# Kernel optimization log

Measured on AMD Instinct MI355X. Metric: run time of the kernel, lower is better.

Reference implementation:

```python
import jax, jax.numpy as jnp
import numpy as np

CUTOFF = 1.0          # nm, PhysNet attenuation cutoff
KE = 138.96           # Coulomb constant in kJ/mol*nm/e^2
N_ATOMS = 245760
N_PAIRS = 16_777_216
N_MOLS = 4096


def physnet_attenuation(r):
    # PhysNet smooth cutoff: 1 - 6u^5 + 15u^4 - 10u^3 for u = r/cutoff < 1, else 0
    u = r / CUTOFF
    phi = 1.0 - 6.0 * u**5 + 15.0 * u**4 - 10.0 * u**3
    return jnp.where(u < 1.0, phi, 0.0)


def setup_inputs() -> dict:
    key = jax.random.key(0)
    k1, k2, k3, k4 = jax.random.split(key, 4)
    per_atom_charge = jax.random.normal(k1, (N_ATOMS,), dtype=jnp.float32) * 0.2
    raw = jax.random.randint(k2, (2, N_PAIRS), 0, N_ATOMS, dtype=jnp.int32)
    # enforce idx_i <= idx_j; equal pairs are dropped by the idx_i < idx_j mask
    pair_indices = jnp.stack([jnp.minimum(raw[0], raw[1]), jnp.maximum(raw[0], raw[1])])
    # distances in (0.05, 1.5) nm to avoid div-by-zero and span the cutoff
    d_ij = jax.random.uniform(k3, (N_PAIRS, 1), dtype=jnp.float32) * 1.45 + 0.05
    atomic_subsystem_indices = jax.random.randint(k4, (N_PAIRS,), 0, N_MOLS, dtype=jnp.int32)
    per_system_energy = jnp.zeros((N_MOLS,), dtype=jnp.float32)
    return {
        "per_atom_charge": per_atom_charge,
        "pair_indices": pair_indices,
        "d_ij": d_ij,
        "atomic_subsystem_indices": atomic_subsystem_indices,
        "per_system_energy": per_system_energy,
    }


def reference(per_atom_charge, pair_indices, d_ij, atomic_subsystem_indices, per_system_energy):
    idx_i = pair_indices[0]
    idx_j = pair_indices[1]
    unique_mask = idx_i < idx_j  # keep each pair once (static-shape masking via where)
    d = d_ij[:, 0]  # [P]
    phi_2r = physnet_attenuation(2.0 * d)
    # cutoff-blended Coulomb kernel chi(r)
    chi_r = phi_2r / jnp.sqrt(d * d + 1.0) + (1.0 - phi_2r) / d
    contrib = per_atom_charge[idx_i] * per_atom_charge[idx_j] * chi_r
    contrib = jnp.where(unique_mask, contrib, 0.0)
    energy = per_system_energy + jax.ops.segment_sum(
        contrib, atomic_subsystem_indices, num_segments=N_MOLS
    )
    return energy * KE
```

## Files before the change

### kernel.cpp

```cpp
#include <hip/hip_runtime.h>

static constexpr int   NPAIRS = 16777216;
static constexpr int   NMOLS  = 4096;
static constexpr float KEF    = 138.96f;
static constexpr int   TPB    = 256;
static constexpr int   BLOCKS = 2048;
static constexpr int   WAVES  = TPB / 64;
static constexpr int   NITER  = NPAIRS / 4 / (BLOCKS * TPB);

typedef int   vi4 __attribute__((ext_vector_type(4)));
typedef float vf4 __attribute__((ext_vector_type(4)));

__global__ __launch_bounds__(256) void zero_out_kernel(float* __restrict__ out) {
    int i = blockIdx.x * 256 + threadIdx.x;
    if (i < NMOLS) out[i] = 0.0f;
}

__device__ __forceinline__ void stage16(const void* gptr, void* lptr) {
    __builtin_amdgcn_global_load_lds((const unsigned int*)gptr, (unsigned int*)lptr,
                                     16, 0, 0);
}

__device__ __forceinline__ float pair_contrib(const float* __restrict__ q,
                                              int i, int j, float d) {
    float u = 2.0f * d;
    float phi = 0.0f;
    if (u < 1.0f) {
        phi = 1.0f - u * u * u * (10.0f + u * (6.0f * u - 15.0f));
    }
    float rs = __builtin_amdgcn_rsqf(d * d + 1.0f);
    float rd = __builtin_amdgcn_rcpf(d);
    float chi = phi * rs + (1.0f - phi) * rd;
    float c = q[i] * q[j] * chi;
    return (i < j) ? c : 0.0f;
}

__global__ __launch_bounds__(TPB) void coulomb_kernel(
    const float* __restrict__ q,
    const int*   __restrict__ pidx,
    const float* __restrict__ dij,
    const int*   __restrict__ mol,
    float*       __restrict__ out)
{
    __shared__ float bins[NMOLS];
    __shared__ vi4   stage[WAVES][4][64];
    for (int i = threadIdx.x; i < NMOLS; i += TPB) bins[i] = 0.0f;
    __syncthreads();

    const vi4* pi4 = (const vi4*)pidx;
    const vi4* pj4 = (const vi4*)(pidx + NPAIRS);
    const vf4* d4  = (const vf4*)dij;
    const vi4* m4  = (const vi4*)mol;

    const int lane   = threadIdx.x & 63;
    const int wave   = threadIdx.x >> 6;
    const int stride = BLOCKS * TPB;
    int v = blockIdx.x * TPB + threadIdx.x;

    #pragma unroll 1
    for (int k = 0; k < NITER; ++k, v += stride) {
        stage16(&pi4[v], &stage[wave][0][0]);
        stage16(&pj4[v], &stage[wave][1][0]);
        stage16(&d4[v],  &stage[wave][2][0]);
        stage16(&m4[v],  &stage[wave][3][0]);
        asm volatile("s_waitcnt vmcnt(0)" ::: "memory");

        vi4 ii = stage[wave][0][lane];
        vi4 jj = stage[wave][1][lane];
        vf4 dd = (vf4)stage[wave][2][lane];
        vi4 mm = stage[wave][3][lane];

        float c0 = pair_contrib(q, ii.x, jj.x, dd.x);
        float c1 = pair_contrib(q, ii.y, jj.y, dd.y);
        float c2 = pair_contrib(q, ii.z, jj.z, dd.z);
        float c3 = pair_contrib(q, ii.w, jj.w, dd.w);

        atomicAdd(&bins[mm.x], c0);
        atomicAdd(&bins[mm.y], c1);
        atomicAdd(&bins[mm.z], c2);
        atomicAdd(&bins[mm.w], c3);
    }

    __syncthreads();
    for (int i = threadIdx.x; i < NMOLS; i += TPB) {
        atomicAdd(&out[i], bins[i]);
    }
}

__global__ __launch_bounds__(256) void finalize_kernel(float* __restrict__ out,
                                                       const float* __restrict__ pse) {
    int i = blockIdx.x * 256 + threadIdx.x;
    if (i < NMOLS) out[i] = (out[i] + pse[i]) * KEF;
}

extern "C" void kernel_launch(void* const* d_in, const int* in_sizes, int n_in,
                              void* d_out, int out_size, void* d_ws, size_t ws_size,
                              hipStream_t stream) {
    const float* q    = (const float*)d_in[0];
    const int*   pidx = (const int*)  d_in[1];
    const float* dij  = (const float*)d_in[2];
    const int*   mol  = (const int*)  d_in[3];
    const float* pse  = (const float*)d_in[4];
    float* out = (float*)d_out;

    zero_out_kernel<<<NMOLS / 256, 256, 0, stream>>>(out);
    coulomb_kernel<<<BLOCKS, TPB, 0, stream>>>(q, pidx, dij, mol, out);
    finalize_kernel<<<NMOLS / 256, 256, 0, stream>>>(out, pse);
}
```

Measured before the change: 381.0 us.

## Software-pipeline register prefetch of pair streams, drop LDS staging, use 1024-thread blocks

Replaces the per-iteration global_load_lds staging with a full vmcnt(0) wait by register-based software pipelining. Index vectors are prefetched two iterations ahead and distances and molecule ids one iteration ahead, all with nontemporal loads. Block size goes from 256 to 1024 threads with 512 blocks, which cuts the number of per-block LDS histograms to merge. The aim is to overlap the dependent charge gathers with streaming loads, at the cost of higher register pressure and occupancy pressure from the launch_bounds hint.

Result: slower. 393.0 us (+3.2%).

```diff
diff --git a/kernel.cpp b/kernel.cpp
--- a/kernel.cpp
+++ b/kernel.cpp
@@ -3,9 +3,8 @@
 static constexpr int   NPAIRS = 16777216;
 static constexpr int   NMOLS  = 4096;
 static constexpr float KEF    = 138.96f;
-static constexpr int   TPB    = 256;
-static constexpr int   BLOCKS = 2048;
-static constexpr int   WAVES  = TPB / 64;
+static constexpr int   TPB    = 1024;
+static constexpr int   BLOCKS = 512;
 static constexpr int   NITER  = NPAIRS / 4 / (BLOCKS * TPB);
 
 typedef int   vi4 __attribute__((ext_vector_type(4)));
@@ -16,12 +15,7 @@
     if (i < NMOLS) out[i] = 0.0f;
 }
 
-__device__ __forceinline__ void stage16(const void* gptr, void* lptr) {
-    __builtin_amdgcn_global_load_lds((const unsigned int*)gptr, (unsigned int*)lptr,
-                                     16, 0, 0);
-}
-
-__device__ __forceinline__ float pair_contrib(const float* __restrict__ q,
+__device__ __forceinline__ float pair_contrib(float qi, float qj,
                                               int i, int j, float d) {
     float u = 2.0f * d;
     float phi = 0.0f;
@@ -31,11 +25,11 @@
     float rs = __builtin_amdgcn_rsqf(d * d + 1.0f);
     float rd = __builtin_amdgcn_rcpf(d);
     float chi = phi * rs + (1.0f - phi) * rd;
-    float c = q[i] * q[j] * chi;
+    float c = qi * qj * chi;
     return (i < j) ? c : 0.0f;
 }
 
-__global__ __launch_bounds__(TPB) void coulomb_kernel(
+__global__ __launch_bounds__(TPB, 8) void coulomb_kernel(
     const float* __restrict__ q,
     const int*   __restrict__ pidx,
     const float* __restrict__ dij,
@@ -43,7 +37,6 @@
     float*       __restrict__ out)
 {
     __shared__ float bins[NMOLS];
-    __shared__ vi4   stage[WAVES][4][64];
     for (int i = threadIdx.x; i < NMOLS; i += TPB) bins[i] = 0.0f;
     __syncthreads();
 
@@ -52,33 +45,49 @@
     const vf4* d4  = (const vf4*)dij;
     const vi4* m4  = (const vi4*)mol;
 
-    const int lane   = threadIdx.x & 63;
-    const int wave   = threadIdx.x >> 6;
     const int stride = BLOCKS * TPB;
     int v = blockIdx.x * TPB + threadIdx.x;
 
+    vi4 ii0 = __builtin_nontemporal_load(&pi4[v]);
+    vi4 jj0 = __builtin_nontemporal_load(&pj4[v]);
+    vi4 ii1 = __builtin_nontemporal_load(&pi4[v + stride]);
+    vi4 jj1 = __builtin_nontemporal_load(&pj4[v + stride]);
+    vf4 dd0 = __builtin_nontemporal_load(&d4[v]);
+    vi4 mm0 = __builtin_nontemporal_load(&m4[v]);
+
     #pragma unroll 1
-    for (int k = 0; k < NITER; ++k, v += stride) {
-        stage16(&pi4[v], &stage[wave][0][0]);
-        stage16(&pj4[v], &stage[wave][1][0]);
-        stage16(&d4[v],  &stage[wave][2][0]);
-        stage16(&m4[v],  &stage[wave][3][0]);
-        asm volatile("s_waitcnt vmcnt(0)" ::: "memory");
+    for (int k = 0; k < NITER; ++k) {
+        vi4 ii2 = ii1, jj2 = jj1;
+        vf4 dd1 = dd0;
+        vi4 mm1 = mm0;
+        if (k + 2 < NITER) {
+            ii2 = __builtin_nontemporal_load(&pi4[v + 2 * stride]);
+            jj2 = __builtin_nontemporal_load(&pj4[v + 2 * stride]);
+        }
+        if (k + 1 < NITER) {
+            dd1 = __builtin_nontemporal_load(&d4[v + stride]);
+            mm1 = __builtin_nontemporal_load(&m4[v + stride]);
+        }
 
-        vi4 ii = stage[wave][0][lane];
-        vi4 jj = stage[wave][1][lane];
-        vf4 dd = (vf4)stage[wave][2][lane];
-        vi4 mm = stage[wave][3][lane];
+        float qi0 = q[ii0.x], qj0 = q[jj0.x];
+        float qi1 = q[ii0.y], qj1 = q[jj0.y];
+        float qi2 = q[ii0.z], qj2 = q[jj0.z];
+        float qi3 = q[ii0.w], qj3 = q[jj0.w];
 
-        float c0 = pair_contrib(q, ii.x, jj.x, dd.x);
-        float c1 = pair_contrib(q, ii.y, jj.y, dd.y);
-        float c2 = pair_contrib(q, ii.z, jj.z, dd.z);
-        float c3 = pair_contrib(q, ii.w, jj.w, dd.w);
+        float c0 = pair_contrib(qi0, qj0, ii0.x, jj0.x, dd0.x);
+        float c1 = pair_contrib(qi1, qj1, ii0.y, jj0.y, dd0.y);
+        float c2 = pair_contrib(qi2, qj2, ii0.z, jj0.z, dd0.z);
+        float c3 = pair_contrib(qi3, qj3, ii0.w, jj0.w, dd0.w);
 
-        atomicAdd(&bins[mm.x], c0);
-        atomicAdd(&bins[mm.y], c1);
-        atomicAdd(&bins[mm.z], c2);
-        atomicAdd(&bins[mm.w], c3);
+        atomicAdd(&bins[mm0.x], c0);
+        atomicAdd(&bins[mm0.y], c1);
+        atomicAdd(&bins[mm0.z], c2);
+        atomicAdd(&bins[mm0.w], c3);
+
+        ii0 = ii1; jj0 = jj1;
+        ii1 = ii2; jj1 = jj2;
+        dd0 = dd1; mm0 = mm1;
+        v += stride;
     }
 
     __syncthreads();
```
